# Kernel tuning notes

Measured on AMD Instinct MI355X. Metric: run time of the kernel, lower is better.

Reference implementation:

```python
import jax, jax.numpy as jnp
import numpy as np

N = 8192        # nodes
F_IN = 128      # input features (layers_dims[0])
F_OUT = 64      # per-head output features (layers_dims[1])
H = 4           # nheads
ALPHA = 0.2     # leaky relu slope
DENSITY = 0.01  # edge density for the random graph


def setup_inputs() -> dict:
    key = jax.random.key(0)
    kx, ka, kw, k1, k2 = jax.random.split(key, 5)
    x = jax.random.normal(kx, (N, F_IN), dtype=jnp.float32)
    adj = (jax.random.uniform(ka, (N, N)) < DENSITY).astype(jnp.float32)
    adj = jnp.maximum(adj, jnp.eye(N, dtype=jnp.float32))
    W = jax.random.normal(kw, (H, F_IN, F_OUT), dtype=jnp.float32) * (1.0 / np.sqrt(F_IN))
    a1 = jax.random.normal(k1, (H, F_OUT), dtype=jnp.float32) * (1.0 / np.sqrt(F_OUT))
    a2 = jax.random.normal(k2, (H, F_OUT), dtype=jnp.float32) * (1.0 / np.sqrt(F_OUT))
    return {"x": x, "adj": adj, "W": W, "a1": a1, "a2": a2}


def reference(x, adj, W, a1, a2):
    # Dropout layers are identity in eval mode (training=False).
    # Per-head projection: Wh[h] = x @ W[h]  -> [H, N, F_OUT]
    Wh = jnp.einsum('nf,hfo->hno', x, W)
    # e_ij = leakyReLU(a1 . Wh_i + a2 . Wh_j) via rank-1 broadcast (classic GAT trick)
    f1 = jnp.einsum('hno,ho->hn', Wh, a1)   # [H, N] (dst contribution)
    f2 = jnp.einsum('hno,ho->hn', Wh, a2)   # [H, N] (src contribution)
    e = f1[:, :, None] + f2[:, None, :]     # [H, N, N]
    e = jnp.where(e > 0, e, ALPHA * e)      # leaky relu
    # mask non-edges, softmax over neighbors (last axis)
    e = jnp.where(adj[None, :, :] > 0, e, jnp.float32(-1e9))
    att = jax.nn.softmax(e, axis=-1)        # [H, N, N]
    # aggregate and apply elu (concat=True branch)
    out = jnp.einsum('hnm,hmo->hno', att, Wh)  # [H, N, F_OUT]
    out = jax.nn.elu(out)
    # concat heads on feature dim -> [N, H*F_OUT]
    return jnp.transpose(out, (1, 0, 2)).reshape(N, H * F_OUT)
```

## Files before the change

kernel.cpp:

```cpp
#include <hip/hip_runtime.h>
#include <hip/hip_bf16.h>
#include <math.h>

#define N_NODES 8192
#define F_IN    128
#define F_OUT   64
#define NH      4
#define FC      256
#define MAXDEG  512

typedef float f32x4 __attribute__((ext_vector_type(4)));

__global__ __launch_bounds__(256) void k_proj(const float* __restrict__ x,
                                              const float* __restrict__ W,
                                              const float* __restrict__ a1,
                                              const float* __restrict__ a2,
                                              float* __restrict__ Wh,
                                              __hip_bfloat16* __restrict__ Wh16,
                                              float* __restrict__ f1,
                                              float* __restrict__ f2) {
    __shared__ float xs[16][128];
    __shared__ float ws[32][256];
    const int t = threadIdx.x;
    const int row0 = blockIdx.x * 16;

    {
        const float4* xg = (const float4*)(x + (size_t)row0 * F_IN);
        float4* xls = (float4*)&xs[0][0];
        xls[t]       = xg[t];
        xls[t + 256] = xg[t + 256];
    }

    const int tx = t & 63;
    const int ty = t >> 6;
    const int c0 = tx * 4;
    const int r0 = ty * 4;
    const int h  = tx >> 4;

    float acc[4][4];
#pragma unroll
    for (int r = 0; r < 4; r++)
#pragma unroll
        for (int c = 0; c < 4; c++) acc[r][c] = 0.f;

    for (int kt = 0; kt < 4; kt++) {
        __syncthreads();
        for (int q = t; q < 2048; q += 256) {
            int krow = q >> 6;
            int c4 = (q & 63) * 4;
            int hh = c4 >> 6;
            int o  = c4 & 63;
            *(float4*)&ws[krow][c4] =
                *(const float4*)(W + (size_t)hh * (F_IN * F_OUT)
                                   + (size_t)(kt * 32 + krow) * F_OUT + o);
        }
        __syncthreads();
#pragma unroll
        for (int kg = 0; kg < 8; kg++) {
            const int kb = kt * 32 + kg * 4;
            float4 xa0 = *(const float4*)&xs[r0 + 0][kb];
            float4 xa1 = *(const float4*)&xs[r0 + 1][kb];
            float4 xa2 = *(const float4*)&xs[r0 + 2][kb];
            float4 xa3 = *(const float4*)&xs[r0 + 3][kb];
            float a0k[4] = {xa0.x, xa0.y, xa0.z, xa0.w};
            float a1k[4] = {xa1.x, xa1.y, xa1.z, xa1.w};
            float a2k[4] = {xa2.x, xa2.y, xa2.z, xa2.w};
            float a3k[4] = {xa3.x, xa3.y, xa3.z, xa3.w};
#pragma unroll
            for (int kk = 0; kk < 4; kk++) {
                float4 b = *(const float4*)&ws[kg * 4 + kk][c0];
                acc[0][0] += a0k[kk] * b.x; acc[0][1] += a0k[kk] * b.y;
                acc[0][2] += a0k[kk] * b.z; acc[0][3] += a0k[kk] * b.w;
                acc[1][0] += a1k[kk] * b.x; acc[1][1] += a1k[kk] * b.y;
                acc[1][2] += a1k[kk] * b.z; acc[1][3] += a1k[kk] * b.w;
                acc[2][0] += a2k[kk] * b.x; acc[2][1] += a2k[kk] * b.y;
                acc[2][2] += a2k[kk] * b.z; acc[2][3] += a2k[kk] * b.w;
                acc[3][0] += a3k[kk] * b.x; acc[3][1] += a3k[kk] * b.y;
                acc[3][2] += a3k[kk] * b.z; acc[3][3] += a3k[kk] * b.w;
            }
        }
    }

    float a1c[4], a2c[4];
#pragma unroll
    for (int c = 0; c < 4; c++) { a1c[c] = a1[c0 + c]; a2c[c] = a2[c0 + c]; }

#pragma unroll
    for (int r = 0; r < 4; r++) {
        const int row = row0 + r0 + r;
        float4 v = make_float4(acc[r][0], acc[r][1], acc[r][2], acc[r][3]);
        *(float4*)&Wh[(size_t)row * FC + c0] = v;
        union { __hip_bfloat16 hv[4]; uint2 u; } pk;
        pk.hv[0] = __float2bfloat16(v.x); pk.hv[1] = __float2bfloat16(v.y);
        pk.hv[2] = __float2bfloat16(v.z); pk.hv[3] = __float2bfloat16(v.w);
        *(uint2*)(Wh16 + (size_t)row * FC + c0) = pk.u;
        float s1 = acc[r][0] * a1c[0] + acc[r][1] * a1c[1]
                 + acc[r][2] * a1c[2] + acc[r][3] * a1c[3];
        float s2 = acc[r][0] * a2c[0] + acc[r][1] * a2c[1]
                 + acc[r][2] * a2c[2] + acc[r][3] * a2c[3];
#pragma unroll
        for (int d = 1; d < 16; d <<= 1) {
            s1 += __shfl_xor(s1, d, 64);
            s2 += __shfl_xor(s2, d, 64);
        }
        if ((tx & 15) == 0) {
            f1[row * NH + h] = s1;
            f2[row * NH + h] = s2;
        }
    }
}

__global__ __launch_bounds__(256) void k_gat(const float* __restrict__ adj,
                                             const __hip_bfloat16* __restrict__ Wh16,
                                             const float* __restrict__ f1,
                                             const float* __restrict__ f2,
                                             float* __restrict__ out) {
    __shared__ int cnt;
    __shared__ int jlist[MAXDEG];
    __shared__ float pbuf[NH][MAXDEG];

    const int i = blockIdx.x;
    const int t = threadIdx.x;
    if (t == 0) cnt = 0;
    __syncthreads();

    const f32x4* arow = (const f32x4*)(adj + (size_t)i * N_NODES);
    for (int q = t; q < N_NODES / 4; q += 256) {
        f32x4 v = __builtin_nontemporal_load(&arow[q]);
        int jb = q * 4;
        if (v.x > 0.f) { int p = atomicAdd(&cnt, 1); if (p < MAXDEG) jlist[p] = jb; }
        if (v.y > 0.f) { int p = atomicAdd(&cnt, 1); if (p < MAXDEG) jlist[p] = jb + 1; }
        if (v.z > 0.f) { int p = atomicAdd(&cnt, 1); if (p < MAXDEG) jlist[p] = jb + 2; }
        if (v.w > 0.f) { int p = atomicAdd(&cnt, 1); if (p < MAXDEG) jlist[p] = jb + 3; }
    }
    __syncthreads();
    const int deg = min(cnt, MAXDEG);

    const int h = t >> 6;
    const int lane = t & 63;
    const float f1i = f1[i * NH + h];

    float m = -1e30f;
    for (int e = lane; e < deg; e += 64) {
        int j = jlist[e];
        float s = f1i + f2[j * NH + h];
        s = s > 0.f ? s : 0.2f * s;
        pbuf[h][e] = s;
        m = fmaxf(m, s);
    }
#pragma unroll
    for (int d = 32; d > 0; d >>= 1) m = fmaxf(m, __shfl_xor(m, d, 64));

    float l = 0.f;
    for (int e = lane; e < deg; e += 64) {
        float pv = __expf(pbuf[h][e] - m);
        pbuf[h][e] = pv;
        l += pv;
    }
#pragma unroll
    for (int d = 32; d > 0; d >>= 1) l += __shfl_xor(l, d, 64);
    const float inv = 1.f / l;

    float acc0 = 0.f, acc1 = 0.f, acc2 = 0.f, acc3 = 0.f;
    const __hip_bfloat16* whh = Wh16 + h * F_OUT + lane;
    int e = 0;
    for (; e + 4 <= deg; e += 4) {
        int j0 = jlist[e], j1 = jlist[e + 1], j2 = jlist[e + 2], j3 = jlist[e + 3];
        float p0 = pbuf[h][e], p1 = pbuf[h][e + 1];
        float p2 = pbuf[h][e + 2], p3 = pbuf[h][e + 3];
        float w0 = __bfloat162float(whh[(size_t)j0 * FC]);
        float w1 = __bfloat162float(whh[(size_t)j1 * FC]);
        float w2 = __bfloat162float(whh[(size_t)j2 * FC]);
        float w3 = __bfloat162float(whh[(size_t)j3 * FC]);
        acc0 += p0 * w0; acc1 += p1 * w1; acc2 += p2 * w2; acc3 += p3 * w3;
    }
    for (; e < deg; e++)
        acc0 += pbuf[h][e] * __bfloat162float(whh[(size_t)jlist[e] * FC]);

    float v = (acc0 + acc1 + acc2 + acc3) * inv;
    v = v > 0.f ? v : (__expf(v) - 1.f);
    out[(size_t)i * FC + t] = v;
}

extern "C" void kernel_launch(void* const* d_in, const int* in_sizes, int n_in,
                              void* d_out, int out_size, void* d_ws, size_t ws_size,
                              hipStream_t stream) {
    const float* x   = (const float*)d_in[0];
    const float* adj = (const float*)d_in[1];
    const float* W   = (const float*)d_in[2];
    const float* a1  = (const float*)d_in[3];
    const float* a2  = (const float*)d_in[4];
    float* out = (float*)d_out;

    float* Wh = (float*)d_ws;
    __hip_bfloat16* Wh16 = (__hip_bfloat16*)(Wh + (size_t)N_NODES * FC);
    float* f1 = (float*)(Wh16 + (size_t)N_NODES * FC);
    float* f2 = f1 + (size_t)N_NODES * NH;

    k_proj<<<N_NODES / 16, 256, 0, stream>>>(x, W, a1, a2, Wh, Wh16, f1, f2);
    k_gat<<<N_NODES, 256, 0, stream>>>(adj, Wh16, f1, f2, out);
}
```

Before: 412.5 us.

## Drop unused fp32 Wh store, batch adjacency loads, gather bf16 pairs per lane

The projection kernel no longer writes the unused fp32 Wh copy and stores only the bf16 version. In the attention kernel, each thread issues all eight nontemporal adjacency-row loads before scanning them, which raises memory-level parallelism on the dominant 256 MB adjacency read. The aggregation now has each lane load a packed pair of bf16 features as one 32-bit word, with the two half-waves handling alternate neighbors. A cross-half shuffle combines the partial sums, trading more shuffles and a half-idle epilogue for fewer, wider gather loads.

Result: faster. 398.9 us (-3.3%).

```diff
diff --git a/kernel.cpp b/kernel.cpp
--- a/kernel.cpp
+++ b/kernel.cpp
@@ -15,7 +15,6 @@
                                               const float* __restrict__ W,
                                               const float* __restrict__ a1,
                                               const float* __restrict__ a2,
-                                              float* __restrict__ Wh,
                                               __hip_bfloat16* __restrict__ Wh16,
                                               float* __restrict__ f1,
                                               float* __restrict__ f2) {
@@ -88,11 +87,11 @@
 #pragma unroll
     for (int r = 0; r < 4; r++) {
         const int row = row0 + r0 + r;
-        float4 v = make_float4(acc[r][0], acc[r][1], acc[r][2], acc[r][3]);
-        *(float4*)&Wh[(size_t)row * FC + c0] = v;
         union { __hip_bfloat16 hv[4]; uint2 u; } pk;
-        pk.hv[0] = __float2bfloat16(v.x); pk.hv[1] = __float2bfloat16(v.y);
-        pk.hv[2] = __float2bfloat16(v.z); pk.hv[3] = __float2bfloat16(v.w);
+        pk.hv[0] = __float2bfloat16(acc[r][0]);
+        pk.hv[1] = __float2bfloat16(acc[r][1]);
+        pk.hv[2] = __float2bfloat16(acc[r][2]);
+        pk.hv[3] = __float2bfloat16(acc[r][3]);
         *(uint2*)(Wh16 + (size_t)row * FC + c0) = pk.u;
         float s1 = acc[r][0] * a1c[0] + acc[r][1] * a1c[1]
                  + acc[r][2] * a1c[2] + acc[r][3] * a1c[3];
@@ -125,13 +124,17 @@
     __syncthreads();
 
     const f32x4* arow = (const f32x4*)(adj + (size_t)i * N_NODES);
-    for (int q = t; q < N_NODES / 4; q += 256) {
-        f32x4 v = __builtin_nontemporal_load(&arow[q]);
-        int jb = q * 4;
-        if (v.x > 0.f) { int p = atomicAdd(&cnt, 1); if (p < MAXDEG) jlist[p] = jb; }
-        if (v.y > 0.f) { int p = atomicAdd(&cnt, 1); if (p < MAXDEG) jlist[p] = jb + 1; }
-        if (v.z > 0.f) { int p = atomicAdd(&cnt, 1); if (p < MAXDEG) jlist[p] = jb + 2; }
-        if (v.w > 0.f) { int p = atomicAdd(&cnt, 1); if (p < MAXDEG) jlist[p] = jb + 3; }
+    f32x4 v[8];
+#pragma unroll
+    for (int u = 0; u < 8; u++)
+        v[u] = __builtin_nontemporal_load(&arow[t + u * 256]);
+#pragma unroll
+    for (int u = 0; u < 8; u++) {
+        const int jb = (t + u * 256) * 4;
+        if (v[u].x > 0.f) { int p = atomicAdd(&cnt, 1); if (p < MAXDEG) jlist[p] = jb; }
+        if (v[u].y > 0.f) { int p = atomicAdd(&cnt, 1); if (p < MAXDEG) jlist[p] = jb + 1; }
+        if (v[u].z > 0.f) { int p = atomicAdd(&cnt, 1); if (p < MAXDEG) jlist[p] = jb + 2; }
+        if (v[u].w > 0.f) { int p = atomicAdd(&cnt, 1); if (p < MAXDEG) jlist[p] = jb + 3; }
     }
     __syncthreads();
     const int deg = min(cnt, MAXDEG);
@@ -161,25 +164,49 @@
     for (int d = 32; d > 0; d >>= 1) l += __shfl_xor(l, d, 64);
     const float inv = 1.f / l;
 
-    float acc0 = 0.f, acc1 = 0.f, acc2 = 0.f, acc3 = 0.f;
-    const __hip_bfloat16* whh = Wh16 + h * F_OUT + lane;
+    const int fp  = lane & 31;
+    const int sub = lane >> 5;
+    const uint* whu = (const uint*)Wh16 + h * 32 + fp;
+
+    float aA0 = 0.f, aB0 = 0.f, aA1 = 0.f, aB1 = 0.f;
     int e = 0;
     for (; e + 4 <= deg; e += 4) {
-        int j0 = jlist[e], j1 = jlist[e + 1], j2 = jlist[e + 2], j3 = jlist[e + 3];
-        float p0 = pbuf[h][e], p1 = pbuf[h][e + 1];
-        float p2 = pbuf[h][e + 2], p3 = pbuf[h][e + 3];
-        float w0 = __bfloat162float(whh[(size_t)j0 * FC]);
-        float w1 = __bfloat162float(whh[(size_t)j1 * FC]);
-        float w2 = __bfloat162float(whh[(size_t)j2 * FC]);
-        float w3 = __bfloat162float(whh[(size_t)j3 * FC]);
-        acc0 += p0 * w0; acc1 += p1 * w1; acc2 += p2 * w2; acc3 += p3 * w3;
-    }
-    for (; e < deg; e++)
-        acc0 += pbuf[h][e] * __bfloat162float(whh[(size_t)jlist[e] * FC]);
-
-    float v = (acc0 + acc1 + acc2 + acc3) * inv;
-    v = v > 0.f ? v : (__expf(v) - 1.f);
-    out[(size_t)i * FC + t] = v;
+        int j0 = jlist[e + sub];
+        int j1 = jlist[e + 2 + sub];
+        float p0 = pbuf[h][e + sub];
+        float p1 = pbuf[h][e + 2 + sub];
+        uint w0 = whu[(size_t)j0 * 128];
+        uint w1 = whu[(size_t)j1 * 128];
+        aA0 += p0 * __uint_as_float(w0 << 16);
+        aB0 += p0 * __uint_as_float(w0 & 0xffff0000u);
+        aA1 += p1 * __uint_as_float(w1 << 16);
+        aB1 += p1 * __uint_as_float(w1 & 0xffff0000u);
+    }
+    for (; e + 2 <= deg; e += 2) {
+        int j = jlist[e + sub];
+        float p = pbuf[h][e + sub];
+        uint w = whu[(size_t)j * 128];
+        aA0 += p * __uint_as_float(w << 16);
+        aB0 += p * __uint_as_float(w & 0xffff0000u);
+    }
+    if (e < deg && sub == 0) {
+        int j = jlist[e];
+        float p = pbuf[h][e];
+        uint w = whu[(size_t)j * 128];
+        aA0 += p * __uint_as_float(w << 16);
+        aB0 += p * __uint_as_float(w & 0xffff0000u);
+    }
+    float accA = aA0 + aA1, accB = aB0 + aB1;
+    accA += __shfl_xor(accA, 32, 64);
+    accB += __shfl_xor(accB, 32, 64);
+
+    if (sub == 0) {
+        float sA = accA * inv, sB = accB * inv;
+        float2 r;
+        r.x = sA > 0.f ? sA : (__expf(sA) - 1.f);
+        r.y = sB > 0.f ? sB : (__expf(sB) - 1.f);
+        *(float2*)&out[(size_t)i * FC + h * F_OUT + fp * 2] = r;
+    }
 }
 
 extern "C" void kernel_launch(void* const* d_in, const int* in_sizes, int n_in,
@@ -192,11 +219,10 @@
     const float* a2  = (const float*)d_in[4];
     float* out = (float*)d_out;
 
-    float* Wh = (float*)d_ws;
-    __hip_bfloat16* Wh16 = (__hip_bfloat16*)(Wh + (size_t)N_NODES * FC);
+    __hip_bfloat16* Wh16 = (__hip_bfloat16*)d_ws;
     float* f1 = (float*)(Wh16 + (size_t)N_NODES * FC);
     float* f2 = f1 + (size_t)N_NODES * NH;
 
-    k_proj<<<N_NODES / 16, 256, 0, stream>>>(x, W, a1, a2, Wh, Wh16, f1, f2);
+    k_proj<<<N_NODES / 16, 256, 0, stream>>>(x, W, a1, a2, Wh16, f1, f2);
     k_gat<<<N_NODES, 256, 0, stream>>>(adj, Wh16, f1, f2, out);
 }
```
